# Optimization experiments

Measured on AMD Instinct MI355X. Metric: run time of the kernel, lower is better.

## Reference

```python
import jax, jax.numpy as jnp
import numpy as np

B, S, D_DIM = 32, 512, 1024

def setup_inputs() -> dict:
    key = jax.random.key(0)
    k1, k2, k3, k4 = jax.random.split(key, 4)
    return {
        "D": jax.random.normal(k1, (B, S, D_DIM), dtype=jnp.float32),
        "H": jax.random.normal(k2, (B, S, D_DIM), dtype=jnp.float32),
        # learned params: U is (d+1, d) (xavier-style scale), W is (2d+1,)
        # (original inits W to zeros; we use small random values so the linear
        #  term is exercised — same math either way)
        "U": jax.random.normal(k3, (D_DIM + 1, D_DIM), dtype=jnp.float32) * 0.02,
        "W": jax.random.normal(k4, (2 * D_DIM + 1,), dtype=jnp.float32) * 0.02,
    }

def reference(D, H, U, W):
    # D, H: [B, S, d]; U: [d+1, d]; W: [2d+1]
    d = H.shape[-1]
    ones = jnp.ones(D.shape[:2] + (1,), dtype=D.dtype)
    Daug = jnp.concatenate([D, ones], axis=-1)              # [B, S, d+1]
    # bilinear term: v.U.u  -> [B, Sx, Sy]
    bil = jnp.einsum('bxi,ij,byj->bxy', Daug, U, H)
    # linear term W . concat(D_aug, H): algebraically split — avoids the
    # O(B*S*S*2d) concatenated intermediate of the original implementation
    lin = (Daug @ W[:d + 1])[:, :, None] + (H @ W[d + 1:])[:, None, :]
    return bil + lin
```

## Files before the change

### kernel.cpp

```cpp
#include <hip/hip_runtime.h>


#define D_DIM 1024
#define ROWS 16384

typedef float floatx4 __attribute__((ext_vector_type(4)));
typedef __bf16 bf16x8 __attribute__((ext_vector_type(8)));

__device__ inline unsigned short f2bf(float f) {
  unsigned int u = __builtin_bit_cast(unsigned int, f);
  u = (u + 0x7FFFu + ((u >> 16) & 1u)) >> 16;
  return (unsigned short)u;
}

__device__ inline void async_load16(const void* g, void* l) {
  __builtin_amdgcn_global_load_lds(
      (const __attribute__((address_space(1))) void*)g,
      (__attribute__((address_space(3))) void*)l, 16, 0, 0);
}

__global__ __launch_bounds__(256) void cast_rows_kernel(
    const float* __restrict__ D, const float* __restrict__ H,
    const float* __restrict__ W,
    unsigned short* __restrict__ Dbf, unsigned short* __restrict__ Hbf,
    float* __restrict__ linD, float* __restrict__ linH) {
  int rowid = blockIdx.x;
  bool isH = rowid >= ROWS;
  int r = isH ? rowid - ROWS : rowid;
  const float* src = (isH ? H : D) + (size_t)r * D_DIM;
  unsigned short* dst = (isH ? Hbf : Dbf) + (size_t)r * D_DIM;
  const float* w = W + (isH ? (D_DIM + 1) : 0);
  int t = threadIdx.x;
  float4 v = ((const float4*)src)[t];
  float s = v.x * w[4*t] + v.y * w[4*t+1] + v.z * w[4*t+2] + v.w * w[4*t+3];
  ushort4 o;
  o.x = f2bf(v.x); o.y = f2bf(v.y); o.z = f2bf(v.z); o.w = f2bf(v.w);
  ((ushort4*)dst)[t] = o;
  #pragma unroll
  for (int off = 32; off > 0; off >>= 1) s += __shfl_down(s, off, 64);
  __shared__ float red[4];
  int wave = t >> 6;
  if ((t & 63) == 0) red[wave] = s;
  __syncthreads();
  if (t == 0) {
    float tot = red[0] + red[1] + red[2] + red[3];
    if (!isH) tot += W[D_DIM];
    (isH ? linH : linD)[r] = tot;
  }
}

__global__ __launch_bounds__(256) void transU_kernel(
    const float* __restrict__ U, unsigned short* __restrict__ Ut) {
  __shared__ float tile[32][33];
  int n0 = blockIdx.x * 32;
  int k0 = blockIdx.y * 32;
  int t = threadIdx.x;
  int tr = t >> 5, tc = t & 31;
  #pragma unroll
  for (int i = 0; i < 32; i += 8)
    tile[tr + i][tc] = U[(size_t)(k0 + tr + i) * D_DIM + n0 + tc];
  __syncthreads();
  #pragma unroll
  for (int i = 0; i < 32; i += 8)
    Ut[(size_t)(n0 + tr + i) * D_DIM + k0 + tc] = f2bf(tile[tc][tr + i]);
}

__global__ __launch_bounds__(256) void gemm1_kernel(
    const unsigned short* __restrict__ A,
    const unsigned short* __restrict__ Bt,
    const float* __restrict__ Ubias,
    unsigned short* __restrict__ T) {
  __shared__ __align__(16) unsigned short As[128 * 32];
  __shared__ __align__(16) unsigned short Bs[128 * 32];
  const int K = D_DIM;
  int tid = threadIdx.x;
  int lane = tid & 63, wave = tid >> 6;
  int quad = lane >> 4, lrow = lane & 15;
  int wm = wave >> 1, wn = wave & 1;
  int m0 = blockIdx.y * 128, n0 = blockIdx.x * 128;

  floatx4 acc[4][4] = {};

  int cc0 = tid, cc1 = tid + 256;
  int r0 = cc0 >> 2, kc0 = (cc0 & 3) * 8;
  int r1 = cc1 >> 2, kc1 = (cc1 & 3) * 8;
  const unsigned short* gA0 = A + (size_t)(m0 + r0) * K + kc0;
  const unsigned short* gA1 = A + (size_t)(m0 + r1) * K + kc1;
  const unsigned short* gB0 = Bt + (size_t)(n0 + r0) * K + kc0;
  const unsigned short* gB1 = Bt + (size_t)(n0 + r1) * K + kc1;

  for (int k0 = 0; k0 < K; k0 += 32) {
    __syncthreads();
    async_load16(gA0 + k0, As + cc0 * 8);
    async_load16(gA1 + k0, As + cc1 * 8);
    async_load16(gB0 + k0, Bs + cc0 * 8);
    async_load16(gB1 + k0, Bs + cc1 * 8);
    __syncthreads();
    bf16x8 a[4], b[4];
    #pragma unroll
    for (int mt = 0; mt < 4; ++mt)
      a[mt] = *(const bf16x8*)(As + (wm * 64 + mt * 16 + lrow) * 32 + quad * 8);
    #pragma unroll
    for (int nt = 0; nt < 4; ++nt)
      b[nt] = *(const bf16x8*)(Bs + (wn * 64 + nt * 16 + lrow) * 32 + quad * 8);
    #pragma unroll
    for (int mt = 0; mt < 4; ++mt)
      #pragma unroll
      for (int nt = 0; nt < 4; ++nt)
        acc[mt][nt] = __builtin_amdgcn_mfma_f32_16x16x32_bf16(
            a[mt], b[nt], acc[mt][nt], 0, 0, 0);
  }
  #pragma unroll
  for (int mt = 0; mt < 4; ++mt)
    #pragma unroll
    for (int nt = 0; nt < 4; ++nt) {
      int row = m0 + wm * 64 + mt * 16 + quad * 4;
      int col = n0 + wn * 64 + nt * 16 + lrow;
      float bias = Ubias[col];
      #pragma unroll
      for (int rr = 0; rr < 4; ++rr)
        T[(size_t)(row + rr) * D_DIM + col] = f2bf(acc[mt][nt][rr] + bias);
    }
}

__global__ __launch_bounds__(256) void gemm2_kernel(
    const unsigned short* __restrict__ Tg,
    const unsigned short* __restrict__ Hbf,
    const float* __restrict__ linD, const float* __restrict__ linH,
    float* __restrict__ out) {
  __shared__ __align__(16) unsigned short As[128 * 32];
  __shared__ __align__(16) unsigned short Bs[128 * 32];
  const int K = D_DIM;
  int tid = threadIdx.x;
  int lane = tid & 63, wave = tid >> 6;
  int quad = lane >> 4, lrow = lane & 15;
  int wm = wave >> 1, wn = wave & 1;
  int b = blockIdx.z;
  int m0 = blockIdx.y * 128, n0 = blockIdx.x * 128;
  const unsigned short* A = Tg + (size_t)b * 512 * D_DIM;
  const unsigned short* Bt = Hbf + (size_t)b * 512 * D_DIM;

  floatx4 acc[4][4] = {};

  int cc0 = tid, cc1 = tid + 256;
  int r0 = cc0 >> 2, kc0 = (cc0 & 3) * 8;
  int r1 = cc1 >> 2, kc1 = (cc1 & 3) * 8;
  const unsigned short* gA0 = A + (size_t)(m0 + r0) * K + kc0;
  const unsigned short* gA1 = A + (size_t)(m0 + r1) * K + kc1;
  const unsigned short* gB0 = Bt + (size_t)(n0 + r0) * K + kc0;
  const unsigned short* gB1 = Bt + (size_t)(n0 + r1) * K + kc1;

  for (int k0 = 0; k0 < K; k0 += 32) {
    __syncthreads();
    async_load16(gA0 + k0, As + cc0 * 8);
    async_load16(gA1 + k0, As + cc1 * 8);
    async_load16(gB0 + k0, Bs + cc0 * 8);
    async_load16(gB1 + k0, Bs + cc1 * 8);
    __syncthreads();
    bf16x8 a[4], bfr[4];
    #pragma unroll
    for (int mt = 0; mt < 4; ++mt)
      a[mt] = *(const bf16x8*)(As + (wm * 64 + mt * 16 + lrow) * 32 + quad * 8);
    #pragma unroll
    for (int nt = 0; nt < 4; ++nt)
      bfr[nt] = *(const bf16x8*)(Bs + (wn * 64 + nt * 16 + lrow) * 32 + quad * 8);
    #pragma unroll
    for (int mt = 0; mt < 4; ++mt)
      #pragma unroll
      for (int nt = 0; nt < 4; ++nt)
        acc[mt][nt] = __builtin_amdgcn_mfma_f32_16x16x32_bf16(
            a[mt], bfr[nt], acc[mt][nt], 0, 0, 0);
  }
  #pragma unroll
  for (int mt = 0; mt < 4; ++mt)
    #pragma unroll
    for (int nt = 0; nt < 4; ++nt) {
      int row = m0 + wm * 64 + mt * 16 + quad * 4;
      int col = n0 + wn * 64 + nt * 16 + lrow;
      float lh = linH[b * 512 + col];
      #pragma unroll
      for (int rr = 0; rr < 4; ++rr) {
        float v = acc[mt][nt][rr] + linD[b * 512 + row + rr] + lh;
        out[((size_t)b * 512 + row + rr) * 512 + col] = v;
      }
    }
}

extern "C" void kernel_launch(void* const* d_in, const int* in_sizes, int n_in,
                              void* d_out, int out_size, void* d_ws, size_t ws_size,
                              hipStream_t stream) {
  const float* D = (const float*)d_in[0];
  const float* H = (const float*)d_in[1];
  const float* U = (const float*)d_in[2];
  const float* W = (const float*)d_in[3];
  float* out = (float*)d_out;

  char* ws = (char*)d_ws;
  unsigned short* Dbf = (unsigned short*)ws; ws += (size_t)ROWS * D_DIM * 2;
  unsigned short* Hbf = (unsigned short*)ws; ws += (size_t)ROWS * D_DIM * 2;
  unsigned short* Tbf = (unsigned short*)ws; ws += (size_t)ROWS * D_DIM * 2;
  unsigned short* Ut  = (unsigned short*)ws; ws += (size_t)D_DIM * D_DIM * 2;
  float* linD = (float*)ws;                  ws += (size_t)ROWS * 4;
  float* linH = (float*)ws;                  ws += (size_t)ROWS * 4;

  cast_rows_kernel<<<dim3(2 * ROWS), 256, 0, stream>>>(D, H, W, Dbf, Hbf, linD, linH);
  transU_kernel<<<dim3(32, 32), 256, 0, stream>>>(U, Ut);
  gemm1_kernel<<<dim3(8, 128), 256, 0, stream>>>(Dbf, Ut, U + (size_t)D_DIM * D_DIM, Tbf);
  gemm2_kernel<<<dim3(4, 4, 32), 256, 0, stream>>>(Tbf, Hbf, linD, linH, out);
}
```

Baseline: 251.8 us.

## Double K-tile depth, use k-major LDS layout, and remap GEMM grid order

Both GEMMs now load a 64-deep K slice per iteration instead of 32, halving the number of barrier pairs per tile. The LDS layout becomes k-chunk-major (chunk index times 128 rows), so the 16-byte fragment reads for each MFMA step are contiguous across lanes, which should reduce bank conflicts. The grid is also reordered so consecutive blocks walk along M (gemm1) or along the batch (gemm2), which changes L2 reuse of the shared operand. LDS use doubles to 32 KB per block, which may lower occupancy.

```diff
diff --git a/kernel.cpp b/kernel.cpp
--- a/kernel.cpp
+++ b/kernel.cpp
@@ -65,51 +65,64 @@
     Ut[(size_t)(n0 + tr + i) * D_DIM + k0 + tc] = f2bf(tile[tc][tr + i]);
 }
 
+__device__ inline void gemm_core_128(
+    const unsigned short* __restrict__ A, const unsigned short* __restrict__ Bt,
+    int m0, int n0, unsigned short* As, unsigned short* Bs,
+    floatx4 (&acc)[4][4]) {
+  const int K = D_DIM;
+  int tid = threadIdx.x;
+  int lane = tid & 63, wave = tid >> 6;
+  int quad = lane >> 4, lrow = lane & 15;
+  int wm = wave >> 1, wn = wave & 1;
+
+  int q0 = tid >> 7;
+  int rr0 = tid & 127;
+  const unsigned short* gA = A + (size_t)(m0 + rr0) * K + q0 * 8;
+  const unsigned short* gB = Bt + (size_t)(n0 + rr0) * K + q0 * 8;
+
+  for (int k0 = 0; k0 < K; k0 += 64) {
+    __syncthreads();
+    #pragma unroll
+    for (int i = 0; i < 4; ++i) {
+      async_load16(gA + k0 + i * 16, As + (i * 256 + tid) * 8);
+      async_load16(gB + k0 + i * 16, Bs + (i * 256 + tid) * 8);
+    }
+    __syncthreads();
+    #pragma unroll
+    for (int s = 0; s < 2; ++s) {
+      bf16x8 a[4], b[4];
+      #pragma unroll
+      for (int mt = 0; mt < 4; ++mt)
+        a[mt] = *(const bf16x8*)(As + (((s * 4 + quad) * 128) + wm * 64 + mt * 16 + lrow) * 8);
+      #pragma unroll
+      for (int nt = 0; nt < 4; ++nt)
+        b[nt] = *(const bf16x8*)(Bs + (((s * 4 + quad) * 128) + wn * 64 + nt * 16 + lrow) * 8);
+      #pragma unroll
+      for (int mt = 0; mt < 4; ++mt)
+        #pragma unroll
+        for (int nt = 0; nt < 4; ++nt)
+          acc[mt][nt] = __builtin_amdgcn_mfma_f32_16x16x32_bf16(
+              a[mt], b[nt], acc[mt][nt], 0, 0, 0);
+    }
+  }
+}
+
 __global__ __launch_bounds__(256) void gemm1_kernel(
     const unsigned short* __restrict__ A,
     const unsigned short* __restrict__ Bt,
     const float* __restrict__ Ubias,
     unsigned short* __restrict__ T) {
-  __shared__ __align__(16) unsigned short As[128 * 32];
-  __shared__ __align__(16) unsigned short Bs[128 * 32];
-  const int K = D_DIM;
+  __shared__ __align__(16) unsigned short As[128 * 64];
+  __shared__ __align__(16) unsigned short Bs[128 * 64];
+  int m0 = blockIdx.x * 128, n0 = blockIdx.y * 128;
   int tid = threadIdx.x;
   int lane = tid & 63, wave = tid >> 6;
   int quad = lane >> 4, lrow = lane & 15;
   int wm = wave >> 1, wn = wave & 1;
-  int m0 = blockIdx.y * 128, n0 = blockIdx.x * 128;
 
   floatx4 acc[4][4] = {};
+  gemm_core_128(A, Bt, m0, n0, As, Bs, acc);
 
-  int cc0 = tid, cc1 = tid + 256;
-  int r0 = cc0 >> 2, kc0 = (cc0 & 3) * 8;
-  int r1 = cc1 >> 2, kc1 = (cc1 & 3) * 8;
-  const unsigned short* gA0 = A + (size_t)(m0 + r0) * K + kc0;
-  const unsigned short* gA1 = A + (size_t)(m0 + r1) * K + kc1;
-  const unsigned short* gB0 = Bt + (size_t)(n0 + r0) * K + kc0;
-  const unsigned short* gB1 = Bt + (size_t)(n0 + r1) * K + kc1;
-
-  for (int k0 = 0; k0 < K; k0 += 32) {
-    __syncthreads();
-    async_load16(gA0 + k0, As + cc0 * 8);
-    async_load16(gA1 + k0, As + cc1 * 8);
-    async_load16(gB0 + k0, Bs + cc0 * 8);
-    async_load16(gB1 + k0, Bs + cc1 * 8);
-    __syncthreads();
-    bf16x8 a[4], b[4];
-    #pragma unroll
-    for (int mt = 0; mt < 4; ++mt)
-      a[mt] = *(const bf16x8*)(As + (wm * 64 + mt * 16 + lrow) * 32 + quad * 8);
-    #pragma unroll
-    for (int nt = 0; nt < 4; ++nt)
-      b[nt] = *(const bf16x8*)(Bs + (wn * 64 + nt * 16 + lrow) * 32 + quad * 8);
-    #pragma unroll
-    for (int mt = 0; mt < 4; ++mt)
-      #pragma unroll
-      for (int nt = 0; nt < 4; ++nt)
-        acc[mt][nt] = __builtin_amdgcn_mfma_f32_16x16x32_bf16(
-            a[mt], b[nt], acc[mt][nt], 0, 0, 0);
-  }
   #pragma unroll
   for (int mt = 0; mt < 4; ++mt)
     #pragma unroll
@@ -128,49 +141,21 @@
     const unsigned short* __restrict__ Hbf,
     const float* __restrict__ linD, const float* __restrict__ linH,
     float* __restrict__ out) {
-  __shared__ __align__(16) unsigned short As[128 * 32];
-  __shared__ __align__(16) unsigned short Bs[128 * 32];
-  const int K = D_DIM;
+  __shared__ __align__(16) unsigned short As[128 * 64];
+  __shared__ __align__(16) unsigned short Bs[128 * 64];
+  int b = blockIdx.x;
+  int t = blockIdx.y;
+  int m0 = (t >> 2) * 128, n0 = (t & 3) * 128;
+  const unsigned short* A = Tg + (size_t)b * 512 * D_DIM;
+  const unsigned short* Bt = Hbf + (size_t)b * 512 * D_DIM;
   int tid = threadIdx.x;
   int lane = tid & 63, wave = tid >> 6;
   int quad = lane >> 4, lrow = lane & 15;
   int wm = wave >> 1, wn = wave & 1;
-  int b = blockIdx.z;
-  int m0 = blockIdx.y * 128, n0 = blockIdx.x * 128;
-  const unsigned short* A = Tg + (size_t)b * 512 * D_DIM;
-  const unsigned short* Bt = Hbf + (size_t)b * 512 * D_DIM;
 
   floatx4 acc[4][4] = {};
+  gemm_core_128(A, Bt, m0, n0, As, Bs, acc);
 
-  int cc0 = tid, cc1 = tid + 256;
-  int r0 = cc0 >> 2, kc0 = (cc0 & 3) * 8;
-  int r1 = cc1 >> 2, kc1 = (cc1 & 3) * 8;
-  const unsigned short* gA0 = A + (size_t)(m0 + r0) * K + kc0;
-  const unsigned short* gA1 = A + (size_t)(m0 + r1) * K + kc1;
-  const unsigned short* gB0 = Bt + (size_t)(n0 + r0) * K + kc0;
-  const unsigned short* gB1 = Bt + (size_t)(n0 + r1) * K + kc1;
-
-  for (int k0 = 0; k0 < K; k0 += 32) {
-    __syncthreads();
-    async_load16(gA0 + k0, As + cc0 * 8);
-    async_load16(gA1 + k0, As + cc1 * 8);
-    async_load16(gB0 + k0, Bs + cc0 * 8);
-    async_load16(gB1 + k0, Bs + cc1 * 8);
-    __syncthreads();
-    bf16x8 a[4], bfr[4];
-    #pragma unroll
-    for (int mt = 0; mt < 4; ++mt)
-      a[mt] = *(const bf16x8*)(As + (wm * 64 + mt * 16 + lrow) * 32 + quad * 8);
-    #pragma unroll
-    for (int nt = 0; nt < 4; ++nt)
-      bfr[nt] = *(const bf16x8*)(Bs + (wn * 64 + nt * 16 + lrow) * 32 + quad * 8);
-    #pragma unroll
-    for (int mt = 0; mt < 4; ++mt)
-      #pragma unroll
-      for (int nt = 0; nt < 4; ++nt)
-        acc[mt][nt] = __builtin_amdgcn_mfma_f32_16x16x32_bf16(
-            a[mt], bfr[nt], acc[mt][nt], 0, 0, 0);
-  }
   #pragma unroll
   for (int mt = 0; mt < 4; ++mt)
     #pragma unroll
@@ -205,6 +190,6 @@
 
   cast_rows_kernel<<<dim3(2 * ROWS), 256, 0, stream>>>(D, H, W, Dbf, Hbf, linD, linH);
   transU_kernel<<<dim3(32, 32), 256, 0, stream>>>(U, Ut);
-  gemm1_kernel<<<dim3(8, 128), 256, 0, stream>>>(Dbf, Ut, U + (size_t)D_DIM * D_DIM, Tbf);
-  gemm2_kernel<<<dim3(4, 4, 32), 256, 0, stream>>>(Tbf, Hbf, linD, linH, out);
+  gemm1_kernel<<<dim3(128, 8), 256, 0, stream>>>(Dbf, Ut, U + (size_t)D_DIM * D_DIM, Tbf);
+  gemm2_kernel<<<dim3(32, 16), 256, 0, stream>>>(Tbf, Hbf, linD, linH, out);
 }
```

New measurement: 278.9 us. +10.8%, slower.
